# Kernel optimization log

Measured on AMD Instinct MI355X. Metric: run time of the kernel, lower is better.

## Reference

```python
import jax, jax.numpy as jnp
import numpy as np

WIN = 4
HEAD_DIM = 32
N_HEADS = 6
TYPE = 'SW'
SHIFT = WIN // 2  # window_size // 2


def _relation():
    # [P, P, 3] relative coordinate indices into the (2w-1)^3 bias table
    cord = np.array([[i, j, k] for i in range(WIN) for j in range(WIN) for k in range(WIN)])
    return cord[:, None, :] - cord[None, :, :] + WIN - 1


def _shift_mask(nw):
    # boolean mask [nw^3, P, P]; True -> -inf (cross-boundary pairs in shifted windows)
    p, s = WIN, WIN - SHIFT
    m = np.zeros((nw, nw, nw, p, p, p, p, p, p), dtype=bool)
    m[-1, :, :, :s, :, :, s:, :, :] = True
    m[-1, :, :, s:, :, :, :s, :, :] = True
    m[:, -1, :, :, :s, :, :, s:, :] = True
    m[:, -1, :, :, s:, :, :, :s, :] = True
    m[:, :, -1, :, :, :s, :, :, s:] = True
    m[:, :, -1, :, :, s:, :, :, :s] = True
    return m.reshape(nw ** 3, p ** 3, p ** 3)


def setup_inputs() -> dict:
    key = jax.random.key(0)
    ks = jax.random.split(key, 6)
    dim = N_HEADS * HEAD_DIM  # 192
    B, S = 2, 32
    x = jax.random.normal(ks[0], (B, S, S, S, dim), jnp.float32)
    W_qkv = jax.random.normal(ks[1], (dim, 3 * dim), jnp.float32) * 0.02
    b_qkv = jnp.zeros((3 * dim,), jnp.float32)
    rel_params = jax.random.normal(ks[2], (N_HEADS, 2 * WIN - 1, 2 * WIN - 1, 2 * WIN - 1), jnp.float32) * 0.02
    W_out = jax.random.normal(ks[3], (dim, dim), jnp.float32) * 0.02
    b_out = jnp.zeros((dim,), jnp.float32)
    return {"x": x, "W_qkv": W_qkv, "b_qkv": b_qkv, "rel_params": rel_params, "W_out": W_out, "b_out": b_out}


def reference(x, W_qkv, b_qkv, rel_params, W_out, b_out):
    B, H, Wd, D, C = x.shape
    p = WIN
    nw = H // p
    scale = HEAD_DIM ** -0.5
    if TYPE != 'W':
        x = jnp.roll(x, (-SHIFT, -SHIFT, -SHIFT), axis=(1, 2, 3))
    # window partition: [B, NW, P, C], NW = nw^3, P = p^3
    xw = x.reshape(B, nw, p, nw, p, nw, p, C).transpose(0, 1, 3, 5, 2, 4, 6, 7).reshape(B, nw ** 3, p ** 3, C)
    qkv = xw @ W_qkv + b_qkv  # [B, NW, P, 3C]
    qkv = qkv.reshape(B, nw ** 3, p ** 3, 3 * N_HEADS, HEAD_DIM).transpose(3, 0, 1, 2, 4)  # [3h, B, NW, P, d]
    q, k, v = qkv[:N_HEADS], qkv[N_HEADS:2 * N_HEADS], qkv[2 * N_HEADS:]
    sim = jnp.einsum('hbwpc,hbwqc->hbwpq', q, k) * scale
    rel = _relation()
    bias = rel_params[:, rel[:, :, 0], rel[:, :, 1], rel[:, :, 2]]  # [h, P, P]
    sim = sim + bias[:, None, None, :, :]
    if TYPE != 'W':
        mask = jnp.asarray(_shift_mask(nw))[None, None]  # [1,1,NW,P,P]
        sim = jnp.where(mask, -jnp.inf, sim)
    probs = jax.nn.softmax(sim, axis=-1)
    out = jnp.einsum('hbwpq,hbwqc->hbwpc', probs, v)
    out = out.transpose(1, 2, 3, 0, 4).reshape(B, nw ** 3, p ** 3, C)  # h b w p c -> b w p (h c)
    out = out @ W_out + b_out
    out = out.reshape(B, nw, nw, nw, p, p, p, C).transpose(0, 1, 4, 2, 5, 3, 6, 7).reshape(B, H, Wd, D, C)
    if TYPE != 'W':
        out = jnp.roll(out, (SHIFT, SHIFT, SHIFT), axis=(1, 2, 3))
    return out
```

## Files before the change

### kernel.cpp

```cpp
#include <hip/hip_runtime.h>

typedef short bf16x8 __attribute__((ext_vector_type(8)));
typedef float f32x4 __attribute__((ext_vector_type(4)));

#define MFMA16(a, b, c) __builtin_amdgcn_mfma_f32_16x16x32_bf16(a, b, c, 0, 0, 0)

__device__ __forceinline__ unsigned short f2bf(float f) {
    unsigned int u = __float_as_uint(f);
    u += 0x7FFFu + ((u >> 16) & 1u);
    return (unsigned short)(u >> 16);
}
__device__ __forceinline__ unsigned int f2bf2(float a, float b) {
    unsigned int ua = __float_as_uint(a);
    ua += 0x7FFFu + ((ua >> 16) & 1u);
    unsigned int ub = __float_as_uint(b);
    ub += 0x7FFFu + ((ub >> 16) & 1u);
    return (ua >> 16) | (ub & 0xFFFF0000u);
}
#define DPPADD(v, CTRL)                                                        \
    {                                                                          \
        int _t = __builtin_amdgcn_mov_dpp(__float_as_int(v), CTRL, 0xf, 0xf, true); \
        v += __int_as_float(_t);                                               \
    }

#define WQT_OFF 0
#define WOT_OFF 221184
#define BQ_OFF  294912
#define TBL_OFF 297216

__global__ void prep_kernel(const float* __restrict__ Wqkv,
                            const float* __restrict__ bqkv,
                            const float* __restrict__ Wout,
                            const float* __restrict__ rel,
                            unsigned short* __restrict__ WqT,
                            unsigned short* __restrict__ WoT,
                            float* __restrict__ bq,
                            float* __restrict__ tblB) {
    __shared__ float tile[32][33];
    const float LOG2E = 1.4426950408889634f;
    const float SCALE = 0.17677669529663687f * 1.4426950408889634f;
    int bid = blockIdx.x;
    int tx = threadIdx.x & 31, ty = threadIdx.x >> 5;
    if (bid < 108) {
        int tn = bid % 18, tc = bid / 18;
#pragma unroll
        for (int i = 0; i < 4; ++i)
            tile[ty + i * 8][tx] = Wqkv[(tc * 32 + ty + i * 8) * 576 + tn * 32 + tx];
        __syncthreads();
        bool isQ = (tn < 6);
#pragma unroll
        for (int i = 0; i < 4; ++i) {
            float v = tile[tx][ty + i * 8];
            if (isQ) v *= SCALE;
            WqT[(tn * 32 + ty + i * 8) * 192 + tc * 32 + tx] = f2bf(v);
        }
    } else if (bid < 144) {
        int bb = bid - 108;
        int tn = bb % 6, tc = bb / 6;
#pragma unroll
        for (int i = 0; i < 4; ++i)
            tile[ty + i * 8][tx] = Wout[(tc * 32 + ty + i * 8) * 192 + tn * 32 + tx];
        __syncthreads();
#pragma unroll
        for (int i = 0; i < 4; ++i)
            WoT[(tn * 32 + ty + i * 8) * 192 + tc * 32 + tx] = f2bf(tile[tx][ty + i * 8]);
    } else if (bid == 144) {
        for (int i = threadIdx.x; i < 576; i += 256) {
            float v = bqkv[i];
            if (i < 192) v *= SCALE;
            bq[i] = v;
        }
    } else {
        int e = (bid - 145) * 256 + threadIdx.x;
        int r = e & 3, f = (e >> 2) & 3;
        int lane = (e >> 4) & 63, mb = (e >> 10) & 3, h = e >> 12;
        int g = lane >> 4, l15 = lane & 15;
        int qy = l15 >> 2, qx = l15 & 3;
        int dz = mb - f + 3, dy = g - qy + 3, dx = r - qx + 3;
        tblB[e] = rel[((h * 7 + dz) * 7 + dy) * 7 + dx] * LOG2E;
    }
}

#define OFF_X   0
#define OFF_P   0
#define OFF_QK  12288
#define OFF_VT  37376
#define OFF_O   51200
#define SMEM_US 64512

__global__ __launch_bounds__(512, 2) void wmsa_kernel(
    const float* __restrict__ x, const float* __restrict__ tblB,
    const float* __restrict__ bout,
    const unsigned short* __restrict__ WqT,
    const unsigned short* __restrict__ WoT,
    const float* __restrict__ bq, float* __restrict__ out) {
    __shared__ __align__(16) unsigned short smem[SMEM_US];

    const int tid = threadIdx.x;
    const int bw = blockIdx.x;
    const int b  = bw >> 9;
    const int w  = bw & 511;
    const int wz = w >> 6, wy = (w >> 3) & 7, wx = w & 7;

    const int lane = tid & 63;
    const int wv   = tid >> 6;
    const int g    = lane >> 4;
    const int l15  = lane & 15;

    {
        int t = tid >> 3, q8 = tid & 7;
        int tz = t >> 4, ty = (t >> 2) & 3, tx = t & 3;
        int gz = (wz * 4 + tz + 2) & 31;
        int gy = (wy * 4 + ty + 2) & 31;
        int gx = (wx * 4 + tx + 2) & 31;
        const float* xp = x + ((((b * 32 + gz) * 32 + gy) * 32 + gx)) * 192;
        int g0 = q8 >> 1, j0 = (q8 & 1) * 4, lt = t & 15;
#pragma unroll
        for (int k = 0; k < 6; ++k) {
            float4 v = *(const float4*)(xp + q8 * 4 + k * 32);
            uint2 pk;
            pk.x = f2bf2(v.x, v.y);
            pk.y = f2bf2(v.z, v.w);
            *(uint2*)&smem[OFF_X + ((((k * 4 + g0) * 4 + tz) * 16 + lt) * 8) + j0] = pk;
        }
    }

    int nb = wv;
    float4 bq4 = *(const float4*)&bq[nb * 16 + g * 4];
    float biasv = 0.f;
    bf16x8 bfr[6];
    {
        const unsigned short* wp = WqT + (nb * 16 + l15) * 192 + g * 8;
#pragma unroll
        for (int kk = 0; kk < 6; ++kk) bfr[kk] = *(const bf16x8*)(wp + kk * 32);
    }
    __syncthreads();

    {
        bf16x8 afr[4][6];
#pragma unroll
        for (int m = 0; m < 4; ++m)
#pragma unroll
            for (int kk = 0; kk < 6; ++kk)
                afr[m][kk] = *(const bf16x8*)&smem[OFF_X + (((kk * 4 + g) * 4 + m) * 16 + l15) * 8];

        while (true) {
            int nbN = nb + 8;
            bool more = (nbN < 36);
            bf16x8 bfrN[6];
            float4 bq4N;
            float biasvN = 0.f;
            if (more) {
                if (nbN < 24) bq4N = *(const float4*)&bq[nbN * 16 + g * 4];
                else          biasvN = bq[nbN * 16 + l15];
                const unsigned short* wp = WqT + (nbN * 16 + l15) * 192 + g * 8;
#pragma unroll
                for (int kk = 0; kk < 6; ++kk) bfrN[kk] = *(const bf16x8*)(wp + kk * 32);
            }
            if (nb < 24) {
                int colbase = nb * 16 + g * 4;
#pragma unroll
                for (int m = 0; m < 4; ++m) {
                    f32x4 acc = {bq4.x, bq4.y, bq4.z, bq4.w};
#pragma unroll
                    for (int kk = 0; kk < 6; ++kk) acc = MFMA16(bfr[kk], afr[m][kk], acc);
                    uint2 pk;
                    pk.x = f2bf2(acc[0], acc[1]);
                    pk.y = f2bf2(acc[2], acc[3]);
                    *(uint2*)&smem[OFF_QK + (m * 16 + l15) * 392 + colbase] = pk;
                }
            } else {
                int colg = nb * 16 + l15;
#pragma unroll
                for (int m = 0; m < 4; ++m) {
                    f32x4 acc = {biasv, biasv, biasv, biasv};
#pragma unroll
                    for (int kk = 0; kk < 6; ++kk) acc = MFMA16(afr[m][kk], bfr[kk], acc);
                    int row0 = m * 16 + g * 4;
                    uint2 pk;
                    pk.x = f2bf2(acc[0], acc[1]);
                    pk.y = f2bf2(acc[2], acc[3]);
                    *(uint2*)&smem[OFF_VT + (colg - 384) * 72 + row0] = pk;
                }
            }
            if (!more) break;
            nb = nbN;
            if (nb < 24) bq4 = bq4N; else biasv = biasvN;
#pragma unroll
            for (int kk = 0; kk < 6; ++kk) bfr[kk] = bfrN[kk];
        }
    }
    __syncthreads();

    const bool sz = (wz == 7), sy = (wy == 7), sx = (wx == 7);
    const bool anym = sz | sy | sx;
    {
        const int qy = l15 >> 2, qx = l15 & 3;
        const bool my = sy && ((g < 2) != (qy < 2));
        bool mxr[4];
#pragma unroll
        for (int r = 0; r < 4; ++r) mxr[r] = sx && ((r < 2) != (qx < 2));
        unsigned short* pb = &smem[OFF_P + wv * 1152];
        const int it0 = wv * 3;
        int h = it0 >> 2, mb = it0 & 3;

        bf16x8 qf, kf[4];
        f32x4 bv[4];
        {
            const f32x4* tp = (const f32x4*)(tblB + ((h * 4 + mb) * 64 + lane) * 16);
#pragma unroll
            for (int f = 0; f < 4; ++f) bv[f] = tp[f];
            qf = *(const bf16x8*)&smem[OFF_QK + (mb * 16 + l15) * 392 + h * 32 + g * 8];
#pragma unroll
            for (int f = 0; f < 4; ++f)
                kf[f] = *(const bf16x8*)&smem[OFF_QK + (f * 16 + l15) * 392 + 192 + h * 32 + g * 8];
        }

#pragma unroll
        for (int ii = 0; ii < 3; ++ii) {
            bf16x8 qfN, kfN[4];
            f32x4 bvN[4];
            if (ii < 2) {
                int itN = it0 + ii + 1;
                int hN = itN >> 2, mbN = itN & 3;
                const f32x4* tp = (const f32x4*)(tblB + ((hN * 4 + mbN) * 64 + lane) * 16);
#pragma unroll
                for (int f = 0; f < 4; ++f) bvN[f] = tp[f];
                qfN = *(const bf16x8*)&smem[OFF_QK + (mbN * 16 + l15) * 392 + hN * 32 + g * 8];
#pragma unroll
                for (int f = 0; f < 4; ++f)
                    kfN[f] = *(const bf16x8*)&smem[OFF_QK + (f * 16 + l15) * 392 + 192 + hN * 32 + g * 8];
            }
            const int vtb = OFF_VT + (h * 32 + l15) * 72 + g * 8;
            bf16x8 v00 = *(const bf16x8*)&smem[vtb];
            bf16x8 v01 = *(const bf16x8*)&smem[vtb + 32];
            bf16x8 v10 = *(const bf16x8*)&smem[vtb + 16 * 72];
            bf16x8 v11 = *(const bf16x8*)&smem[vtb + 16 * 72 + 32];

            f32x4 s[4];
#pragma unroll
            for (int f = 0; f < 4; ++f) {
                f32x4 z = {0.f, 0.f, 0.f, 0.f};
                s[f] = MFMA16(qf, kf[f], z);
            }
            if (!anym) {
#pragma unroll
                for (int f = 0; f < 4; ++f)
#pragma unroll
                    for (int r = 0; r < 4; ++r)
                        s[f][r] = exp2f(s[f][r] + bv[f][r]);
            } else {
#pragma unroll
                for (int f = 0; f < 4; ++f) {
                    bool mzy = (sz && ((mb < 2) != (f < 2))) | my;
#pragma unroll
                    for (int r = 0; r < 4; ++r) {
                        float v = s[f][r] + bv[f][r];
                        v = (mzy | mxr[r]) ? -1e30f : v;
                        s[f][r] = exp2f(v);
                    }
                }
            }
            float sm4[4];
#pragma unroll
            for (int r = 0; r < 4; ++r) {
                float sm = (s[0][r] + s[1][r]) + (s[2][r] + s[3][r]);
                DPPADD(sm, 0xB1);
                DPPADD(sm, 0x4E);
                DPPADD(sm, 0x124);
                DPPADD(sm, 0x128);
                sm4[r] = sm;
            }
            const int rq = l15 & 3;
            float ssel = sm4[0];
            ssel = (rq == 1) ? sm4[1] : ssel;
            ssel = (rq == 2) ? sm4[2] : ssel;
            ssel = (rq == 3) ? sm4[3] : ssel;
            float vsel = __builtin_amdgcn_rcpf(ssel);
            if (l15 < 4) *(float*)&pb[(g * 4 + l15) * 72 + 64] = vsel;
#pragma unroll
            for (int f = 0; f < 4; ++f) {
                unsigned int u01 = f2bf2(s[f][0], s[f][1]);
                unsigned int u23 = f2bf2(s[f][2], s[f][3]);
                unsigned short* pw = &pb[(g * 4) * 72 + f * 16 + l15];
                pw[0]   = (unsigned short)u01;
                pw[72]  = (unsigned short)(u01 >> 16);
                pw[144] = (unsigned short)u23;
                pw[216] = (unsigned short)(u23 >> 16);
            }
            float invq = *(float*)&pb[l15 * 72 + 64];
            bf16x8 pf0 = *(const bf16x8*)&pb[l15 * 72 + g * 8];
            bf16x8 pf1 = *(const bf16x8*)&pb[l15 * 72 + 32 + g * 8];
            f32x4 o0 = {0.f, 0.f, 0.f, 0.f}, o1 = {0.f, 0.f, 0.f, 0.f};
            o0 = MFMA16(v00, pf0, o0);
            o1 = MFMA16(v10, pf0, o1);
            o0 = MFMA16(v01, pf1, o0);
            o1 = MFMA16(v11, pf1, o1);
#pragma unroll
            for (int r = 0; r < 4; ++r) { o0[r] *= invq; o1[r] *= invq; }
            unsigned short* ow = &smem[OFF_O + (mb * 16 + l15) * 208 + h * 32 + g * 4];
            uint2 pa;
            pa.x = f2bf2(o0[0], o0[1]);
            pa.y = f2bf2(o0[2], o0[3]);
            *(uint2*)ow = pa;
            uint2 pc;
            pc.x = f2bf2(o1[0], o1[1]);
            pc.y = f2bf2(o1[2], o1[3]);
            *(uint2*)(ow + 16) = pc;
            if (ii < 2) {
                int itN = it0 + ii + 1;
                h = itN >> 2; mb = itN & 3;
                qf = qfN;
#pragma unroll
                for (int f = 0; f < 4; ++f) { kf[f] = kfN[f]; bv[f] = bvN[f]; }
            }
        }
    }

    const int mw = wv >> 2, nq = wv & 3;
    int col0 = nq * 16 + l15;
    float boc = bout[col0];
    bf16x8 bfr3[6];
    {
        const unsigned short* wp = WoT + col0 * 192 + g * 8;
#pragma unroll
        for (int kk = 0; kk < 6; ++kk) bfr3[kk] = *(const bf16x8*)(wp + kk * 32);
    }
    __syncthreads();

    {
        bf16x8 ofr[2][6];
#pragma unroll
        for (int mi = 0; mi < 2; ++mi)
#pragma unroll
            for (int kk = 0; kk < 6; ++kk)
                ofr[mi][kk] = *(const bf16x8*)&smem[OFF_O + ((mw * 2 + mi) * 16 + l15) * 208 + kk * 32 + g * 8];
#pragma unroll
        for (int nbi = 0; nbi < 3; ++nbi) {
            int col = (nq + nbi * 4) * 16 + l15;
            float boN = 0.f;
            bf16x8 bfrN[6];
            if (nbi < 2) {
                int colN = (nq + (nbi + 1) * 4) * 16 + l15;
                boN = bout[colN];
                const unsigned short* wp = WoT + colN * 192 + g * 8;
#pragma unroll
                for (int kk = 0; kk < 6; ++kk) bfrN[kk] = *(const bf16x8*)(wp + kk * 32);
            }
#pragma unroll
            for (int mi = 0; mi < 2; ++mi) {
                f32x4 acc = {boc, boc, boc, boc};
#pragma unroll
                for (int kk = 0; kk < 6; ++kk) acc = MFMA16(ofr[mi][kk], bfr3[kk], acc);
                int m = mw * 2 + mi;
                int gz = (wz * 4 + m + 2) & 31;
                int gy = (wy * 4 + g + 2) & 31;
#pragma unroll
                for (int r = 0; r < 4; ++r) {
                    int gx = (wx * 4 + r + 2) & 31;
                    out[(((b * 32 + gz) * 32 + gy) * 32 + gx) * 192 + col] = acc[r];
                }
            }
            boc = boN;
#pragma unroll
            for (int kk = 0; kk < 6; ++kk) bfr3[kk] = bfrN[kk];
        }
    }
}

extern "C" void kernel_launch(void* const* d_in, const int* in_sizes, int n_in,
                              void* d_out, int out_size, void* d_ws, size_t ws_size,
                              hipStream_t stream) {
    const float* x    = (const float*)d_in[0];
    const float* Wqkv = (const float*)d_in[1];
    const float* bqkv = (const float*)d_in[2];
    const float* rel  = (const float*)d_in[3];
    const float* Wout = (const float*)d_in[4];
    const float* bout = (const float*)d_in[5];

    unsigned short* WqT = (unsigned short*)((char*)d_ws + WQT_OFF);
    unsigned short* WoT = (unsigned short*)((char*)d_ws + WOT_OFF);
    float*          bq  = (float*)((char*)d_ws + BQ_OFF);
    float*          tbl = (float*)((char*)d_ws + TBL_OFF);
    float*          out = (float*)d_out;

    prep_kernel<<<241, 256, 0, stream>>>(Wqkv, bqkv, Wout, rel, WqT, WoT, bq, tbl);
    wmsa_kernel<<<1024, 512, 0, stream>>>(x, tbl, bout, WqT, WoT, bq, out);
}
```

Before: 163.6 us.

## Process heads in three two-head passes to shrink LDS and raise occupancy

Restructures the fused window attention kernel so QKV projection, attention and output projection run in three passes of two heads each. The output projection accumulates partial K-slices in registers across passes. This cuts shared memory per block roughly in half so launch bounds can ask for four blocks per CU instead of two. In exchange it adds more barriers, re-reads the X fragments from LDS each pass, loads weights with less prefetch, and raises register pressure from the persistent output accumulators.

```diff
diff --git a/kernel.cpp b/kernel.cpp
--- a/kernel.cpp
+++ b/kernel.cpp
@@ -82,13 +82,13 @@
 }
 
 #define OFF_X   0
-#define OFF_P   0
-#define OFF_QK  12288
-#define OFF_VT  37376
-#define OFF_O   51200
-#define SMEM_US 64512
-
-__global__ __launch_bounds__(512, 2) void wmsa_kernel(
+#define OFF_P   12288
+#define OFF_QK  21504
+#define OFF_VT  30208
+#define OFF_O   34816
+#define SMEM_US 39424
+
+__global__ __launch_bounds__(512, 4) void wmsa_kernel(
     const float* __restrict__ x, const float* __restrict__ tblB,
     const float* __restrict__ bout,
     const unsigned short* __restrict__ WqT,
@@ -125,245 +125,226 @@
         }
     }
 
-    int nb = wv;
-    float4 bq4 = *(const float4*)&bq[nb * 16 + g * 4];
-    float biasv = 0.f;
-    bf16x8 bfr[6];
+    const int lnA = wv;
+    const int mw = wv >> 2, nq = wv & 3;
+    bf16x8 bfrA[6];
+    float4 bq4A;
+    f32x4 bv[4];
+    f32x4 acc3[3][2];
+#pragma unroll
+    for (int nbi = 0; nbi < 3; ++nbi) {
+        float bo = bout[(nq + nbi * 4) * 16 + l15];
+        acc3[nbi][0] = f32x4{bo, bo, bo, bo};
+        acc3[nbi][1] = f32x4{bo, bo, bo, bo};
+    }
     {
-        const unsigned short* wp = WqT + (nb * 16 + l15) * 192 + g * 8;
-#pragma unroll
-        for (int kk = 0; kk < 6; ++kk) bfr[kk] = *(const bf16x8*)(wp + kk * 32);
-    }
-    __syncthreads();
-
+        int rb = (lnA < 4) ? (lnA * 16) : (192 + (lnA - 4) * 16);
+        bq4A = *(const float4*)&bq[rb + g * 4];
+        const unsigned short* wp = WqT + (rb + l15) * 192 + g * 8;
+#pragma unroll
+        for (int kk = 0; kk < 6; ++kk) bfrA[kk] = *(const bf16x8*)(wp + kk * 32);
+    }
+
+    const bool sz = (wz == 7), sy = (wy == 7), sx = (wx == 7);
+    const bool anym = sz | sy | sx;
+    const int qy = l15 >> 2, qx = l15 & 3;
+    const bool my = sy && ((g < 2) != (qy < 2));
+    bool mxr[4], mzy4[4];
     {
+        const int mb = wv & 3;
+#pragma unroll
+        for (int r = 0; r < 4; ++r) mxr[r] = sx && ((r < 2) != (qx < 2));
+#pragma unroll
+        for (int f = 0; f < 4; ++f) mzy4[f] = (sz && ((mb < 2) != (f < 2))) | my;
+    }
+
+    auto ph1 = [&](int p, bool loadA) {
+        if (loadA) {
+            int rb = (lnA < 4) ? (p * 64 + lnA * 16) : (192 + p * 64 + (lnA - 4) * 16);
+            bq4A = *(const float4*)&bq[rb + g * 4];
+            const unsigned short* wp = WqT + (rb + l15) * 192 + g * 8;
+#pragma unroll
+            for (int kk = 0; kk < 6; ++kk) bfrA[kk] = *(const bf16x8*)(wp + kk * 32);
+        }
         bf16x8 afr[4][6];
 #pragma unroll
         for (int m = 0; m < 4; ++m)
 #pragma unroll
             for (int kk = 0; kk < 6; ++kk)
                 afr[m][kk] = *(const bf16x8*)&smem[OFF_X + (((kk * 4 + g) * 4 + m) * 16 + l15) * 8];
-
-        while (true) {
-            int nbN = nb + 8;
-            bool more = (nbN < 36);
-            bf16x8 bfrN[6];
-            float4 bq4N;
-            float biasvN = 0.f;
-            if (more) {
-                if (nbN < 24) bq4N = *(const float4*)&bq[nbN * 16 + g * 4];
-                else          biasvN = bq[nbN * 16 + l15];
-                const unsigned short* wp = WqT + (nbN * 16 + l15) * 192 + g * 8;
-#pragma unroll
-                for (int kk = 0; kk < 6; ++kk) bfrN[kk] = *(const bf16x8*)(wp + kk * 32);
+        {
+            int colbase = ((lnA < 4) ? lnA * 16 : 64 + (lnA - 4) * 16) + g * 4;
+#pragma unroll
+            for (int m = 0; m < 4; ++m) {
+                f32x4 acc = {bq4A.x, bq4A.y, bq4A.z, bq4A.w};
+#pragma unroll
+                for (int kk = 0; kk < 6; ++kk) acc = MFMA16(bfrA[kk], afr[m][kk], acc);
+                uint2 pk;
+                pk.x = f2bf2(acc[0], acc[1]);
+                pk.y = f2bf2(acc[2], acc[3]);
+                *(uint2*)&smem[OFF_QK + (m * 16 + l15) * 136 + colbase] = pk;
             }
-            if (nb < 24) {
-                int colbase = nb * 16 + g * 4;
-#pragma unroll
-                for (int m = 0; m < 4; ++m) {
-                    f32x4 acc = {bq4.x, bq4.y, bq4.z, bq4.w};
-#pragma unroll
-                    for (int kk = 0; kk < 6; ++kk) acc = MFMA16(bfr[kk], afr[m][kk], acc);
-                    uint2 pk;
-                    pk.x = f2bf2(acc[0], acc[1]);
-                    pk.y = f2bf2(acc[2], acc[3]);
-                    *(uint2*)&smem[OFF_QK + (m * 16 + l15) * 392 + colbase] = pk;
+        }
+        if (wv < 4) {
+            int rb = 384 + p * 64 + wv * 16;
+            float biasv = bq[rb + l15];
+            const unsigned short* wp = WqT + (rb + l15) * 192 + g * 8;
+            bf16x8 bfrV[6];
+#pragma unroll
+            for (int kk = 0; kk < 6; ++kk) bfrV[kk] = *(const bf16x8*)(wp + kk * 32);
+#pragma unroll
+            for (int m = 0; m < 4; ++m) {
+                f32x4 acc = {biasv, biasv, biasv, biasv};
+#pragma unroll
+                for (int kk = 0; kk < 6; ++kk) acc = MFMA16(afr[m][kk], bfrV[kk], acc);
+                uint2 pk;
+                pk.x = f2bf2(acc[0], acc[1]);
+                pk.y = f2bf2(acc[2], acc[3]);
+                *(uint2*)&smem[OFF_VT + (wv * 16 + l15) * 72 + m * 16 + g * 4] = pk;
+            }
+        }
+        {
+            int h = 2 * p + (wv >> 2);
+            const f32x4* tp = (const f32x4*)(tblB + ((h * 4 + (wv & 3)) * 64 + lane) * 16);
+#pragma unroll
+            for (int f = 0; f < 4; ++f) bv[f] = tp[f];
+        }
+    };
+
+    auto ph2 = [&](int p) {
+        const int hl = wv >> 2, mb = wv & 3;
+        unsigned short* pb = &smem[OFF_P + wv * 1152];
+        bf16x8 qf = *(const bf16x8*)&smem[OFF_QK + (mb * 16 + l15) * 136 + hl * 32 + g * 8];
+        bf16x8 kf[4];
+#pragma unroll
+        for (int f = 0; f < 4; ++f)
+            kf[f] = *(const bf16x8*)&smem[OFF_QK + (f * 16 + l15) * 136 + 64 + hl * 32 + g * 8];
+        const int vtb = OFF_VT + (hl * 32 + l15) * 72 + g * 8;
+        bf16x8 v00 = *(const bf16x8*)&smem[vtb];
+        bf16x8 v01 = *(const bf16x8*)&smem[vtb + 32];
+        bf16x8 v10 = *(const bf16x8*)&smem[vtb + 16 * 72];
+        bf16x8 v11 = *(const bf16x8*)&smem[vtb + 16 * 72 + 32];
+
+        f32x4 s[4];
+#pragma unroll
+        for (int f = 0; f < 4; ++f) {
+            f32x4 z = {0.f, 0.f, 0.f, 0.f};
+            s[f] = MFMA16(qf, kf[f], z);
+        }
+        if (!anym) {
+#pragma unroll
+            for (int f = 0; f < 4; ++f)
+#pragma unroll
+                for (int r = 0; r < 4; ++r)
+                    s[f][r] = exp2f(s[f][r] + bv[f][r]);
+        } else {
+#pragma unroll
+            for (int f = 0; f < 4; ++f)
+#pragma unroll
+                for (int r = 0; r < 4; ++r) {
+                    float v = s[f][r] + bv[f][r];
+                    v = (mzy4[f] | mxr[r]) ? -1e30f : v;
+                    s[f][r] = exp2f(v);
                 }
-            } else {
-                int colg = nb * 16 + l15;
-#pragma unroll
-                for (int m = 0; m < 4; ++m) {
-                    f32x4 acc = {biasv, biasv, biasv, biasv};
-#pragma unroll
-                    for (int kk = 0; kk < 6; ++kk) acc = MFMA16(afr[m][kk], bfr[kk], acc);
-                    int row0 = m * 16 + g * 4;
-                    uint2 pk;
-                    pk.x = f2bf2(acc[0], acc[1]);
-                    pk.y = f2bf2(acc[2], acc[3]);
-                    *(uint2*)&smem[OFF_VT + (colg - 384) * 72 + row0] = pk;
-                }
-            }
-            if (!more) break;
-            nb = nbN;
-            if (nb < 24) bq4 = bq4N; else biasv = biasvN;
-#pragma unroll
-            for (int kk = 0; kk < 6; ++kk) bfr[kk] = bfrN[kk];
-        }
-    }
-    __syncthreads();
-
-    const bool sz = (wz == 7), sy = (wy == 7), sx = (wx == 7);
-    const bool anym = sz | sy | sx;
-    {
-        const int qy = l15 >> 2, qx = l15 & 3;
-        const bool my = sy && ((g < 2) != (qy < 2));
-        bool mxr[4];
-#pragma unroll
-        for (int r = 0; r < 4; ++r) mxr[r] = sx && ((r < 2) != (qx < 2));
-        unsigned short* pb = &smem[OFF_P + wv * 1152];
-        const int it0 = wv * 3;
-        int h = it0 >> 2, mb = it0 & 3;
-
-        bf16x8 qf, kf[4];
-        f32x4 bv[4];
-        {
-            const f32x4* tp = (const f32x4*)(tblB + ((h * 4 + mb) * 64 + lane) * 16);
-#pragma unroll
-            for (int f = 0; f < 4; ++f) bv[f] = tp[f];
-            qf = *(const bf16x8*)&smem[OFF_QK + (mb * 16 + l15) * 392 + h * 32 + g * 8];
-#pragma unroll
-            for (int f = 0; f < 4; ++f)
-                kf[f] = *(const bf16x8*)&smem[OFF_QK + (f * 16 + l15) * 392 + 192 + h * 32 + g * 8];
-        }
-
-#pragma unroll
-        for (int ii = 0; ii < 3; ++ii) {
-            bf16x8 qfN, kfN[4];
-            f32x4 bvN[4];
-            if (ii < 2) {
-                int itN = it0 + ii + 1;
-                int hN = itN >> 2, mbN = itN & 3;
-                const f32x4* tp = (const f32x4*)(tblB + ((hN * 4 + mbN) * 64 + lane) * 16);
-#pragma unroll
-                for (int f = 0; f < 4; ++f) bvN[f] = tp[f];
-                qfN = *(const bf16x8*)&smem[OFF_QK + (mbN * 16 + l15) * 392 + hN * 32 + g * 8];
-#pragma unroll
-                for (int f = 0; f < 4; ++f)
-                    kfN[f] = *(const bf16x8*)&smem[OFF_QK + (f * 16 + l15) * 392 + 192 + hN * 32 + g * 8];
-            }
-            const int vtb = OFF_VT + (h * 32 + l15) * 72 + g * 8;
-            bf16x8 v00 = *(const bf16x8*)&smem[vtb];
-            bf16x8 v01 = *(const bf16x8*)&smem[vtb + 32];
-            bf16x8 v10 = *(const bf16x8*)&smem[vtb + 16 * 72];
-            bf16x8 v11 = *(const bf16x8*)&smem[vtb + 16 * 72 + 32];
-
-            f32x4 s[4];
-#pragma unroll
-            for (int f = 0; f < 4; ++f) {
-                f32x4 z = {0.f, 0.f, 0.f, 0.f};
-                s[f] = MFMA16(qf, kf[f], z);
-            }
-            if (!anym) {
-#pragma unroll
-                for (int f = 0; f < 4; ++f)
-#pragma unroll
-                    for (int r = 0; r < 4; ++r)
-                        s[f][r] = exp2f(s[f][r] + bv[f][r]);
-            } else {
-#pragma unroll
-                for (int f = 0; f < 4; ++f) {
-                    bool mzy = (sz && ((mb < 2) != (f < 2))) | my;
-#pragma unroll
-                    for (int r = 0; r < 4; ++r) {
-                        float v = s[f][r] + bv[f][r];
-                        v = (mzy | mxr[r]) ? -1e30f : v;
-                        s[f][r] = exp2f(v);
-                    }
-                }
-            }
-            float sm4[4];
-#pragma unroll
-            for (int r = 0; r < 4; ++r) {
-                float sm = (s[0][r] + s[1][r]) + (s[2][r] + s[3][r]);
-                DPPADD(sm, 0xB1);
-                DPPADD(sm, 0x4E);
-                DPPADD(sm, 0x124);
-                DPPADD(sm, 0x128);
-                sm4[r] = sm;
-            }
-            const int rq = l15 & 3;
-            float ssel = sm4[0];
-            ssel = (rq == 1) ? sm4[1] : ssel;
-            ssel = (rq == 2) ? sm4[2] : ssel;
-            ssel = (rq == 3) ? sm4[3] : ssel;
-            float vsel = __builtin_amdgcn_rcpf(ssel);
-            if (l15 < 4) *(float*)&pb[(g * 4 + l15) * 72 + 64] = vsel;
-#pragma unroll
-            for (int f = 0; f < 4; ++f) {
-                unsigned int u01 = f2bf2(s[f][0], s[f][1]);
-                unsigned int u23 = f2bf2(s[f][2], s[f][3]);
-                unsigned short* pw = &pb[(g * 4) * 72 + f * 16 + l15];
-                pw[0]   = (unsigned short)u01;
-                pw[72]  = (unsigned short)(u01 >> 16);
-                pw[144] = (unsigned short)u23;
-                pw[216] = (unsigned short)(u23 >> 16);
-            }
-            float invq = *(float*)&pb[l15 * 72 + 64];
-            bf16x8 pf0 = *(const bf16x8*)&pb[l15 * 72 + g * 8];
-            bf16x8 pf1 = *(const bf16x8*)&pb[l15 * 72 + 32 + g * 8];
-            f32x4 o0 = {0.f, 0.f, 0.f, 0.f}, o1 = {0.f, 0.f, 0.f, 0.f};
-            o0 = MFMA16(v00, pf0, o0);
-            o1 = MFMA16(v10, pf0, o1);
-            o0 = MFMA16(v01, pf1, o0);
-            o1 = MFMA16(v11, pf1, o1);
-#pragma unroll
-            for (int r = 0; r < 4; ++r) { o0[r] *= invq; o1[r] *= invq; }
-            unsigned short* ow = &smem[OFF_O + (mb * 16 + l15) * 208 + h * 32 + g * 4];
-            uint2 pa;
-            pa.x = f2bf2(o0[0], o0[1]);
-            pa.y = f2bf2(o0[2], o0[3]);
-            *(uint2*)ow = pa;
-            uint2 pc;
-            pc.x = f2bf2(o1[0], o1[1]);
-            pc.y = f2bf2(o1[2], o1[3]);
-            *(uint2*)(ow + 16) = pc;
-            if (ii < 2) {
-                int itN = it0 + ii + 1;
-                h = itN >> 2; mb = itN & 3;
-                qf = qfN;
-#pragma unroll
-                for (int f = 0; f < 4; ++f) { kf[f] = kfN[f]; bv[f] = bvN[f]; }
-            }
-        }
-    }
-
-    const int mw = wv >> 2, nq = wv & 3;
-    int col0 = nq * 16 + l15;
-    float boc = bout[col0];
-    bf16x8 bfr3[6];
-    {
-        const unsigned short* wp = WoT + col0 * 192 + g * 8;
-#pragma unroll
-        for (int kk = 0; kk < 6; ++kk) bfr3[kk] = *(const bf16x8*)(wp + kk * 32);
-    }
-    __syncthreads();
-
-    {
-        bf16x8 ofr[2][6];
+        }
+        float sm4[4];
+#pragma unroll
+        for (int r = 0; r < 4; ++r) {
+            float sm = (s[0][r] + s[1][r]) + (s[2][r] + s[3][r]);
+            DPPADD(sm, 0xB1);
+            DPPADD(sm, 0x4E);
+            DPPADD(sm, 0x124);
+            DPPADD(sm, 0x128);
+            sm4[r] = sm;
+        }
+        const int rq = l15 & 3;
+        float ssel = sm4[0];
+        ssel = (rq == 1) ? sm4[1] : ssel;
+        ssel = (rq == 2) ? sm4[2] : ssel;
+        ssel = (rq == 3) ? sm4[3] : ssel;
+        float vsel = __builtin_amdgcn_rcpf(ssel);
+        if (l15 < 4) *(float*)&pb[(g * 4 + l15) * 72 + 64] = vsel;
+#pragma unroll
+        for (int f = 0; f < 4; ++f) {
+            unsigned int u01 = f2bf2(s[f][0], s[f][1]);
+            unsigned int u23 = f2bf2(s[f][2], s[f][3]);
+            unsigned short* pw = &pb[(g * 4) * 72 + f * 16 + l15];
+            pw[0]   = (unsigned short)u01;
+            pw[72]  = (unsigned short)(u01 >> 16);
+            pw[144] = (unsigned short)u23;
+            pw[216] = (unsigned short)(u23 >> 16);
+        }
+        float invq = *(float*)&pb[l15 * 72 + 64];
+        bf16x8 pf0 = *(const bf16x8*)&pb[l15 * 72 + g * 8];
+        bf16x8 pf1 = *(const bf16x8*)&pb[l15 * 72 + 32 + g * 8];
+        f32x4 o0 = {0.f, 0.f, 0.f, 0.f}, o1 = {0.f, 0.f, 0.f, 0.f};
+        o0 = MFMA16(v00, pf0, o0);
+        o1 = MFMA16(v10, pf0, o1);
+        o0 = MFMA16(v01, pf1, o0);
+        o1 = MFMA16(v11, pf1, o1);
+#pragma unroll
+        for (int r = 0; r < 4; ++r) { o0[r] *= invq; o1[r] *= invq; }
+        unsigned short* ow = &smem[OFF_O + (mb * 16 + l15) * 72 + hl * 32 + g * 4];
+        uint2 pa;
+        pa.x = f2bf2(o0[0], o0[1]);
+        pa.y = f2bf2(o0[2], o0[3]);
+        *(uint2*)ow = pa;
+        uint2 pc;
+        pc.x = f2bf2(o1[0], o1[1]);
+        pc.y = f2bf2(o1[2], o1[3]);
+        *(uint2*)(ow + 16) = pc;
+    };
+
+    auto ph3a = [&](int p) {
+        bf16x8 ofr[2][2];
 #pragma unroll
         for (int mi = 0; mi < 2; ++mi)
 #pragma unroll
-            for (int kk = 0; kk < 6; ++kk)
-                ofr[mi][kk] = *(const bf16x8*)&smem[OFF_O + ((mw * 2 + mi) * 16 + l15) * 208 + kk * 32 + g * 8];
+            for (int kkl = 0; kkl < 2; ++kkl)
+                ofr[mi][kkl] = *(const bf16x8*)&smem[OFF_O + ((mw * 2 + mi) * 16 + l15) * 72 + kkl * 32 + g * 8];
 #pragma unroll
         for (int nbi = 0; nbi < 3; ++nbi) {
             int col = (nq + nbi * 4) * 16 + l15;
-            float boN = 0.f;
-            bf16x8 bfrN[6];
-            if (nbi < 2) {
-                int colN = (nq + (nbi + 1) * 4) * 16 + l15;
-                boN = bout[colN];
-                const unsigned short* wp = WoT + colN * 192 + g * 8;
-#pragma unroll
-                for (int kk = 0; kk < 6; ++kk) bfrN[kk] = *(const bf16x8*)(wp + kk * 32);
+            const unsigned short* wp = WoT + col * 192 + p * 64 + g * 8;
+            bf16x8 w0 = *(const bf16x8*)wp;
+            bf16x8 w1 = *(const bf16x8*)(wp + 32);
+            acc3[nbi][0] = MFMA16(ofr[0][0], w0, acc3[nbi][0]);
+            acc3[nbi][1] = MFMA16(ofr[1][0], w0, acc3[nbi][1]);
+            acc3[nbi][0] = MFMA16(ofr[0][1], w1, acc3[nbi][0]);
+            acc3[nbi][1] = MFMA16(ofr[1][1], w1, acc3[nbi][1]);
+        }
+    };
+
+    __syncthreads();
+    ph1(0, false);
+    __syncthreads();
+    ph2(0);
+    __syncthreads();
+    ph3a(0);
+    ph1(1, true);
+    __syncthreads();
+    ph2(1);
+    __syncthreads();
+    ph3a(1);
+    ph1(2, true);
+    __syncthreads();
+    ph2(2);
+    __syncthreads();
+    ph3a(2);
+
+#pragma unroll
+    for (int nbi = 0; nbi < 3; ++nbi) {
+        int col = (nq + nbi * 4) * 16 + l15;
+#pragma unroll
+        for (int mi = 0; mi < 2; ++mi) {
+            int m = mw * 2 + mi;
+            int gz = (wz * 4 + m + 2) & 31;
+            int gy = (wy * 4 + g + 2) & 31;
+#pragma unroll
+            for (int r = 0; r < 4; ++r) {
+                int gx = (wx * 4 + r + 2) & 31;
+                out[(((b * 32 + gz) * 32 + gy) * 32 + gx) * 192 + col] = acc3[nbi][mi][r];
             }
-#pragma unroll
-            for (int mi = 0; mi < 2; ++mi) {
-                f32x4 acc = {boc, boc, boc, boc};
-#pragma unroll
-                for (int kk = 0; kk < 6; ++kk) acc = MFMA16(ofr[mi][kk], bfr3[kk], acc);
-                int m = mw * 2 + mi;
-                int gz = (wz * 4 + m + 2) & 31;
-                int gy = (wy * 4 + g + 2) & 31;
-#pragma unroll
-                for (int r = 0; r < 4; ++r) {
-                    int gx = (wx * 4 + r + 2) & 31;
-                    out[(((b * 32 + gz) * 32 + gy) * 32 + gx) * 192 + col] = acc[r];
-                }
-            }
-            boc = boN;
-#pragma unroll
-            for (int kk = 0; kk < 6; ++kk) bfr3[kk] = bfrN[kk];
         }
     }
 }
```

Measured after the change: 194.5 us. +18.9%, slower.
